# Optimization experiments

Hardware: AMD Instinct MI355X
Metric: run time of the kernel (lower is better)

The kernel has to match this reference:

```python
import jax, jax.numpy as jnp
import numpy as np

HIDDEN = 64

def gcn_conv(x, W, b, src, dst, num_nodes):
    # GCNConv: out = D^{-1/2} (A + I) D^{-1/2} (x @ W) + b
    h = x @ W                                            # [N, F_out]
    ones = jnp.ones(src.shape[0], dtype=x.dtype)
    deg = jax.ops.segment_sum(ones, dst, num_segments=num_nodes) + 1.0  # +1 for self-loop
    dinv = jax.lax.rsqrt(deg)                             # deg^{-1/2}, deg >= 1 so safe
    norm = dinv[src] * dinv[dst]                          # [E]
    msgs = h[src] * norm[:, None]                         # [E, F_out]
    agg = jax.ops.segment_sum(msgs, dst, num_segments=num_nodes)
    # self-loop contribution: norm for (i,i) edge = dinv[i]^2
    out = agg + h * (dinv * dinv)[:, None] + b
    return out


def setup_inputs() -> dict:
    key = jax.random.key(0)
    k1, k2, k3, k4, k5 = jax.random.split(key, 5)
    N, F_in, F_out, E = 50000, 256, 128, 1600000
    x = jax.random.normal(k1, (N, F_in), dtype=jnp.float32)
    edge_index = jax.random.randint(k2, (2, E), 0, N, dtype=jnp.int64)
    W1 = jax.random.normal(k3, (F_in, HIDDEN), dtype=jnp.float32) * (1.0 / np.sqrt(F_in))
    b1 = jnp.zeros((HIDDEN,), dtype=jnp.float32)
    W2 = jax.random.normal(k4, (HIDDEN, F_out), dtype=jnp.float32) * (1.0 / np.sqrt(HIDDEN))
    b2 = jnp.zeros((F_out,), dtype=jnp.float32)
    return {"x": x, "edge_index": edge_index, "W1": W1, "b1": b1, "W2": W2, "b2": b2}


def reference(x, edge_index, W1, b1, W2, b2):
    num_nodes = x.shape[0]
    src, dst = edge_index[0], edge_index[1]
    h = gcn_conv(x, W1, b1, src, dst, num_nodes)
    h = jax.nn.relu(h)
    # dropout is identity in eval mode (training=False)
    out = gcn_conv(h, W2, b2, src, dst, num_nodes)
    return out
```

## Files before the change

### kernel.cpp

```cpp
#include <hip/hip_runtime.h>

#define FI 256
#define FH 64
#define FO 128
#define ASORT_CHUNK 2048

typedef __attribute__((ext_vector_type(8))) short bf16x8;
typedef __attribute__((ext_vector_type(4))) float f32x4;

__device__ __forceinline__ ushort f2bf(float x) {
    unsigned b = __float_as_uint(x);
    b += 0x7fffu + ((b >> 16) & 1u);
    return (ushort)(b >> 16);
}
__device__ __forceinline__ float bf2f(ushort u) {
    return __uint_as_float(((unsigned)u) << 16);
}


__global__ void zero_i32(int* __restrict__ p, int n) {
    int i = blockIdx.x * 256 + threadIdx.x;
    if (i < n) p[i] = 0;
}

__global__ void deg_cnt_kernel(const int* __restrict__ dst, int* __restrict__ cnt, int E) {
    int base = blockIdx.x * 1024 + threadIdx.x;
    #pragma unroll
    for (int q = 0; q < 4; ++q) {
        int e = base + q * 256;
        if (e < E) atomicAdd(&cnt[dst[e]], 1);
    }
}

__global__ void dinv_kernel(const int* __restrict__ cnt, float* __restrict__ dinv, int N) {
    int i = blockIdx.x * 256 + threadIdx.x;
    if (i < N) dinv[i] = rsqrtf((float)cnt[i] + 1.0f);
}


__global__ __launch_bounds__(256) void hist_part_kernel(const int* __restrict__ dst,
                                                        int* __restrict__ bucket_cnt, int E) {
    __shared__ int lcnt[256];
    int t = threadIdx.x;
    int base = blockIdx.x * ASORT_CHUNK;
    lcnt[t] = 0;
    __syncthreads();
    #pragma unroll
    for (int j = 0; j < 8; ++j) {
        int e = base + j * 256 + t;
        if (e < E) atomicAdd(&lcnt[((unsigned)dst[e]) >> 8], 1);
    }
    __syncthreads();
    int v = lcnt[t];
    if (v > 0) atomicAdd(&bucket_cnt[t], v);
}

__global__ __launch_bounds__(256) void bucket_scan_kernel(const int* __restrict__ bucket_cnt,
                                                          int* __restrict__ bucket_base,
                                                          int* __restrict__ bucket_pos, int E) {
    __shared__ int sc[256];
    int t = threadIdx.x;
    int sum = bucket_cnt[t];
    sc[t] = sum;
    __syncthreads();
    for (int off = 1; off < 256; off <<= 1) {
        int u = (t >= off) ? sc[t - off] : 0;
        __syncthreads();
        sc[t] += u;
        __syncthreads();
    }
    int excl = sc[t] - sum;
    bucket_base[t] = excl;
    bucket_pos[t]  = excl;
    if (t == 255) bucket_base[256] = sc[255];
}

__global__ __launch_bounds__(256) void binA_kernel(const int* __restrict__ src,
                                                   const int* __restrict__ dst,
                                                   int* __restrict__ bucket_pos,
                                                   unsigned* __restrict__ binned, int E) {
    __shared__ int lcnt[256];
    __shared__ int lbase[256];
    __shared__ int gbase[256];
    __shared__ int sc[256];
    __shared__ unsigned sorted[ASORT_CHUNK];
    int t = threadIdx.x;
    int base = blockIdx.x * ASORT_CHUNK;
    lcnt[t] = 0;
    __syncthreads();
    unsigned pk[8];
    short bb[8];
    short mi[8];
    #pragma unroll
    for (int j = 0; j < 8; ++j) {
        int e = base + j * 256 + t;
        if (e < E) {
            unsigned s = (unsigned)src[e];
            unsigned d = (unsigned)dst[e];
            pk[j] = s | (d << 16);
            int b = (int)(d >> 8);
            bb[j] = (short)b;
            mi[j] = (short)atomicAdd(&lcnt[b], 1);
        } else {
            bb[j] = -1;
        }
    }
    __syncthreads();
    int v = lcnt[t];
    sc[t] = v;
    __syncthreads();
    #pragma unroll
    for (int off = 1; off < 256; off <<= 1) {
        int u = (t >= off) ? sc[t - off] : 0;
        __syncthreads();
        sc[t] += u;
        __syncthreads();
    }
    lbase[t] = sc[t] - v;
    if (v > 0) gbase[t] = atomicAdd(&bucket_pos[t], v);
    __syncthreads();
    #pragma unroll
    for (int j = 0; j < 8; ++j)
        if (bb[j] >= 0) sorted[lbase[(int)bb[j]] + (int)mi[j]] = pk[j];
    int tot = sc[255];
    __syncthreads();
    for (int i = t; i < tot; i += 256) {
        unsigned vv = sorted[i];
        int b = (int)(vv >> 24);
        binned[gbase[b] + (i - lbase[b])] = vv;
    }
}

__global__ __launch_bounds__(256) void binB_kernel(const int* __restrict__ bucket_base,
                                                   const unsigned* __restrict__ binned,
                                                   int* __restrict__ rec4,
                                                   int* __restrict__ row_start,
                                                   int* __restrict__ cnt,
                                                   float* __restrict__ dinv, int N) {
    __shared__ int lcnt[256];
    __shared__ int sc[256];
    __shared__ int lstart[256];
    __shared__ int loff[256];
    int t = threadIdx.x;
    int d0 = blockIdx.x << 8;
    int start = bucket_base[blockIdx.x];
    int end   = bucket_base[blockIdx.x + 1];
    lcnt[t] = 0;
    __syncthreads();
    for (int i = start + t; i < end; i += 256)
        atomicAdd(&lcnt[(binned[i] >> 16) & 0xffu], 1);
    __syncthreads();
    int v = lcnt[t];
    sc[t] = v;
    __syncthreads();
    for (int off = 1; off < 256; off <<= 1) {
        int u = (t >= off) ? sc[t - off] : 0;
        __syncthreads();
        sc[t] += u;
        __syncthreads();
    }
    int st = start + sc[t] - v;
    lstart[t] = st;
    loff[t] = 0;
    if (d0 + t < N) {
        row_start[d0 + t] = st;
        cnt[d0 + t] = v;
        dinv[d0 + t] = rsqrtf((float)v + 1.0f);
    }
    __syncthreads();
    int i = start + t;
    for (; i + 768 < end; i += 1024) {
        unsigned v0 = binned[i];
        unsigned v1 = binned[i + 256];
        unsigned v2 = binned[i + 512];
        unsigned v3 = binned[i + 768];
        int dA = (int)((v0 >> 16) & 0xffu); int kA = atomicAdd(&loff[dA], 1);
        rec4[lstart[dA] + kA] = (int)(v0 & 0xffffu);
        int dB = (int)((v1 >> 16) & 0xffu); int kB = atomicAdd(&loff[dB], 1);
        rec4[lstart[dB] + kB] = (int)(v1 & 0xffffu);
        int dC = (int)((v2 >> 16) & 0xffu); int kC = atomicAdd(&loff[dC], 1);
        rec4[lstart[dC] + kC] = (int)(v2 & 0xffffu);
        int dD = (int)((v3 >> 16) & 0xffu); int kD = atomicAdd(&loff[dD], 1);
        rec4[lstart[dD] + kD] = (int)(v3 & 0xffffu);
    }
    for (; i < end; i += 256) {
        unsigned v4 = binned[i];
        int d = (int)((v4 >> 16) & 0xffu);
        int k = atomicAdd(&loff[d], 1);
        rec4[lstart[d] + k] = (int)(v4 & 0xffffu);
    }
}


#define ACC8(hv, wt)                                                   \
    acc[0] = fmaf(__uint_as_float((hv).x << 16),         wt, acc[0]);  \
    acc[1] = fmaf(__uint_as_float((hv).x & 0xffff0000u), wt, acc[1]);  \
    acc[2] = fmaf(__uint_as_float((hv).y << 16),         wt, acc[2]);  \
    acc[3] = fmaf(__uint_as_float((hv).y & 0xffff0000u), wt, acc[3]);  \
    acc[4] = fmaf(__uint_as_float((hv).z << 16),         wt, acc[4]);  \
    acc[5] = fmaf(__uint_as_float((hv).z & 0xffff0000u), wt, acc[5]);  \
    acc[6] = fmaf(__uint_as_float((hv).w << 16),         wt, acc[6]);  \
    acc[7] = fmaf(__uint_as_float((hv).w & 0xffff0000u), wt, acc[7]);

#define GATHER_CHUNK(OFFS)                                                     \
    for (int c0 = 0; c0 < n; c0 += 64) {                                       \
        int idx_l = c0 + L;                                                    \
        int sreg = node;                                                       \
        float wreg = 0.f;                                                      \
        if (idx_l < n) {                                                       \
            sreg = rec4[beg + idx_l];                                          \
            wreg = dinv[sreg] * dvd;                                           \
        }                                                                      \
        int m = n - c0; if (m > 64) m = 64;                                    \
        int umax = (m + 7) >> 3;                                               \
        uint4 hv[8];                                                           \
        _Pragma("unroll")                                                      \
        for (int u = 0; u < 8; ++u) {                                          \
            if (u < umax) {                                                    \
                int sidx = __shfl(sreg, u * 8 + g, 64);                        \
                hv[u] = *(const uint4*)(hb + (size_t)sidx * 256 + (OFFS) + q * 8); \
            }                                                                  \
        }                                                                      \
        _Pragma("unroll")                                                      \
        for (int u = 0; u < 8; ++u) {                                          \
            if (u < umax) {                                                    \
                float wt = __shfl(wreg, u * 8 + g, 64);                        \
                ACC8(hv[u], wt)                                                \
            }                                                                  \
        }                                                                      \
    }

__global__ void gather_relu_kernel(const int* __restrict__ rec4, const int* __restrict__ row_start,
                                   const int* __restrict__ cnt, const float* __restrict__ dinv,
                                   const float* __restrict__ b1, float* __restrict__ out, int N) {
    int node = blockIdx.x * 4 + (threadIdx.x >> 6);
    if (node >= N) return;
    int L = threadIdx.x & 63;
    int g = L >> 3;
    int q = L & 7;
    const ushort* hb = (const ushort*)out;
    int beg = row_start[node];
    int n   = cnt[node];
    float dvd = dinv[node];
    float acc[8] = {0.f, 0.f, 0.f, 0.f, 0.f, 0.f, 0.f, 0.f};
    GATHER_CHUNK(128)
    #pragma unroll
    for (int off = 8; off < 64; off <<= 1)
        #pragma unroll
        for (int j = 0; j < 8; ++j)
            acc[j] += __shfl_xor(acc[j], off, 64);
    if (L < 8) {
        float dv2 = dvd * dvd;
        uint4 ho = *(const uint4*)(hb + (size_t)node * 256 + 128 + q * 8);
        float4 bl = *(const float4*)&b1[q * 8];
        float4 bh = *(const float4*)&b1[q * 8 + 4];
        float r0 = fmaxf(acc[0] + dv2 * __uint_as_float(ho.x << 16)         + bl.x, 0.f);
        float r1 = fmaxf(acc[1] + dv2 * __uint_as_float(ho.x & 0xffff0000u) + bl.y, 0.f);
        float r2 = fmaxf(acc[2] + dv2 * __uint_as_float(ho.y << 16)         + bl.z, 0.f);
        float r3 = fmaxf(acc[3] + dv2 * __uint_as_float(ho.y & 0xffff0000u) + bl.w, 0.f);
        float r4 = fmaxf(acc[4] + dv2 * __uint_as_float(ho.z << 16)         + bh.x, 0.f);
        float r5 = fmaxf(acc[5] + dv2 * __uint_as_float(ho.z & 0xffff0000u) + bh.y, 0.f);
        float r6 = fmaxf(acc[6] + dv2 * __uint_as_float(ho.w << 16)         + bh.z, 0.f);
        float r7 = fmaxf(acc[7] + dv2 * __uint_as_float(ho.w & 0xffff0000u) + bh.w, 0.f);
        uint4 st;
        st.x = (unsigned)f2bf(r0) | ((unsigned)f2bf(r1) << 16);
        st.y = (unsigned)f2bf(r2) | ((unsigned)f2bf(r3) << 16);
        st.z = (unsigned)f2bf(r4) | ((unsigned)f2bf(r5) << 16);
        st.w = (unsigned)f2bf(r6) | ((unsigned)f2bf(r7) << 16);
        *(uint4*)((ushort*)out + (size_t)node * 256 + 192 + q * 8) = st;
    }
}

__global__ void gather_comb_kernel(const int* __restrict__ rec4, const int* __restrict__ row_start,
                                   const int* __restrict__ cnt, const float* __restrict__ dinv,
                                   float* __restrict__ out, int N) {
    int node = blockIdx.x * 4 + (threadIdx.x >> 6);
    if (node >= N) return;
    int L = threadIdx.x & 63;
    int g = L >> 3;
    int q = L & 7;
    const ushort* hb = (const ushort*)out;
    int beg = row_start[node];
    int n   = cnt[node];
    float dvd = dinv[node];
    float acc[8] = {0.f, 0.f, 0.f, 0.f, 0.f, 0.f, 0.f, 0.f};
    GATHER_CHUNK(192)
    #pragma unroll
    for (int off = 8; off < 64; off <<= 1)
        #pragma unroll
        for (int j = 0; j < 8; ++j)
            acc[j] += __shfl_xor(acc[j], off, 64);
    if (L < 8) {
        float dv2 = dvd * dvd;
        uint4 ho = *(const uint4*)(hb + (size_t)node * 256 + 192 + q * 8);
        float4 o0, o1;
        o0.x = acc[0] + dv2 * __uint_as_float(ho.x << 16);
        o0.y = acc[1] + dv2 * __uint_as_float(ho.x & 0xffff0000u);
        o0.z = acc[2] + dv2 * __uint_as_float(ho.y << 16);
        o0.w = acc[3] + dv2 * __uint_as_float(ho.y & 0xffff0000u);
        o1.x = acc[4] + dv2 * __uint_as_float(ho.z << 16);
        o1.y = acc[5] + dv2 * __uint_as_float(ho.z & 0xffff0000u);
        o1.z = acc[6] + dv2 * __uint_as_float(ho.w << 16);
        o1.w = acc[7] + dv2 * __uint_as_float(ho.w & 0xffff0000u);
        *(float4*)&out[(size_t)node * FO + q * 8]     = o0;
        *(float4*)&out[(size_t)node * FO + q * 8 + 4] = o1;
    }
}


__global__ __launch_bounds__(512) void mm1_mfma(const float* __restrict__ x,
                                                const float* __restrict__ W1,
                                                float* __restrict__ out, int N) {
    __shared__ short bfH[2048 * 8];
    __shared__ short bfL[2048 * 8];
    int tid = threadIdx.x;

    #pragma unroll
    for (int i = 0; i < 8; ++i) {
        int f = i * 512 + tid;
        float4 wv = *(const float4*)&W1[(size_t)f * 4];
        int k  = f >> 4;
        int c4 = f & 15;
        int j  = k & 7;
        int e0 = ((c4 >> 2) * 8 + (k >> 5)) * 64 + ((k >> 3) & 3) * 16 + (c4 & 3) * 4;
        float vv[4] = {wv.x, wv.y, wv.z, wv.w};
        #pragma unroll
        for (int cc = 0; cc < 4; ++cc) {
            ushort h = f2bf(vv[cc]);
            bfH[(e0 + cc) * 8 + j] = (short)h;
            bfL[(e0 + cc) * 8 + j] = (short)f2bf(vv[cc] - bf2f(h));
        }
    }
    __syncthreads();

    int wid = tid >> 6;
    int l   = tid & 63;
    int R0  = blockIdx.x * 128;
    int rowA = R0 + wid * 16 + (l & 15);
    int kg   = l >> 4;
    const float* xr = x + (size_t)rowA * FI;
    bool ok = rowA < N;
    const float4 z4 = make_float4(0.f, 0.f, 0.f, 0.f);

    f32x4 acc[4];
    #pragma unroll
    for (int c = 0; c < 4; ++c) acc[c] = (f32x4){0.f, 0.f, 0.f, 0.f};

    float4 xa = ok ? *(const float4*)&xr[kg * 8]     : z4;
    float4 xb = ok ? *(const float4*)&xr[kg * 8 + 4] : z4;

    #pragma unroll
    for (int t = 0; t < 8; ++t) {
        bf16x8 ah, al;
        {
            float va[8] = {xa.x, xa.y, xa.z, xa.w, xb.x, xb.y, xb.z, xb.w};
            #pragma unroll
            for (int j = 0; j < 8; ++j) {
                ushort h = f2bf(va[j]);
                ah[j] = (short)h;
                al[j] = (short)f2bf(va[j] - bf2f(h));
            }
        }
        if (t < 7) {
            int kb = (t + 1) * 32 + kg * 8;
            xa = ok ? *(const float4*)&xr[kb]     : z4;
            xb = ok ? *(const float4*)&xr[kb + 4] : z4;
        }
        #pragma unroll
        for (int c = 0; c < 4; ++c) {
            int e = (c * 8 + t) * 64 + l;
            bf16x8 bh = *(const bf16x8*)&bfH[e * 8];
            bf16x8 bl = *(const bf16x8*)&bfL[e * 8];
            acc[c] = __builtin_amdgcn_mfma_f32_16x16x32_bf16(ah, bh, acc[c], 0, 0, 0);
            acc[c] = __builtin_amdgcn_mfma_f32_16x16x32_bf16(ah, bl, acc[c], 0, 0, 0);
            acc[c] = __builtin_amdgcn_mfma_f32_16x16x32_bf16(al, bh, acc[c], 0, 0, 0);
        }
    }
    {
        int rbase = R0 + wid * 16 + (l >> 4) * 4;
        #pragma unroll
        for (int r = 0; r < 4; ++r) {
            int row = rbase + r;
            if (row < N) {
                ushort* ob = (ushort*)out + (size_t)row * 256 + 128;
                #pragma unroll
                for (int c = 0; c < 4; ++c)
                    ob[c * 16 + (l & 15)] = f2bf(acc[c][r]);
            }
        }
    }
}

__global__ __launch_bounds__(256) void mm2_tiled(const float* __restrict__ W2,
                                                 const float* __restrict__ b2,
                                                 float* __restrict__ out, int N) {
    __shared__ float xs[64][68];
    __shared__ float ws[64][128];
    int tid = threadIdx.x;
    int R0  = blockIdx.x * 64;
    int ty  = tid >> 4;
    int tx  = tid & 15;

    {
        int sr = tid >> 2;
        int l4 = tid & 3;
        int grow = R0 + sr;
        bool ok = grow < N;
        const float* orow = out + (size_t)grow * FO;
        #pragma unroll
        for (int q = 0; q < 4; ++q) {
            int j0 = (l4 + 4 * q) * 4;
            float4 a = ok ? *(const float4*)&orow[j0] : make_float4(0.f, 0.f, 0.f, 0.f);
            xs[j0 + 0][sr] = a.x;
            xs[j0 + 1][sr] = a.y;
            xs[j0 + 2][sr] = a.z;
            xs[j0 + 3][sr] = a.w;
        }
    }
    #pragma unroll
    for (int q = 0; q < 8; ++q) {
        int f = tid + q * 256;
        *(float4*)&ws[f >> 5][(f & 31) * 4] = *(const float4*)&W2[(size_t)f * 4];
    }
    __syncthreads();

    float acc[4][8];
    #pragma unroll
    for (int i = 0; i < 4; ++i)
        #pragma unroll
        for (int j = 0; j < 8; ++j) acc[i][j] = 0.f;

    #pragma unroll 4
    for (int k = 0; k < FH; ++k) {
        float4 a  = *(const float4*)&xs[k][ty * 4];
        float4 bl = *(const float4*)&ws[k][tx * 4];
        float4 bh = *(const float4*)&ws[k][64 + tx * 4];
        float av[4] = {a.x, a.y, a.z, a.w};
        float bv[8] = {bl.x, bl.y, bl.z, bl.w, bh.x, bh.y, bh.z, bh.w};
        #pragma unroll
        for (int i = 0; i < 4; ++i)
            #pragma unroll
            for (int j = 0; j < 8; ++j)
                acc[i][j] = fmaf(av[i], bv[j], acc[i][j]);
    }

    float4 b2l = *(const float4*)&b2[tx * 4];
    float4 b2h = *(const float4*)&b2[64 + tx * 4];
    #pragma unroll
    for (int i = 0; i < 4; ++i) {
        int row = R0 + ty * 4 + i;
        if (row < N) {
            float* o = out + (size_t)row * FO;
            *(float4*)&o[tx * 4] = make_float4(acc[i][0] + b2l.x, acc[i][1] + b2l.y,
                                               acc[i][2] + b2l.z, acc[i][3] + b2l.w);
            *(float4*)&o[64 + tx * 4] = make_float4(acc[i][4] + b2h.x, acc[i][5] + b2h.y,
                                                    acc[i][6] + b2h.z, acc[i][7] + b2h.w);
        }
    }
}


__global__ void expand_hs1_kernel(float* __restrict__ out, int N) {
    int row = blockIdx.x * 4 + (threadIdx.x >> 6);
    if (row >= N) return;
    int lane = threadIdx.x & 63;
    float v = bf2f(((const ushort*)out)[(size_t)row * 256 + 128 + lane]);
    out[(size_t)row * FO + FH + lane] = v;
}

__global__ void zero_half_kernel(float* __restrict__ out, int half, int N) {
    int i = blockIdx.x * 256 + threadIdx.x;
    if (i >= N * FH) return;
    out[(size_t)(i >> 6) * FO + half + (i & 63)] = 0.f;
}

__global__ void scatter_half_kernel(const int* __restrict__ src, const int* __restrict__ dst,
                                    const float* __restrict__ dinv, float* __restrict__ out,
                                    int rh, int wh, int E) {
    int e = blockIdx.x * 4 + (threadIdx.x >> 6);
    if (e >= E) return;
    int lane = threadIdx.x & 63;
    int s = src[e];
    int d = dst[e];
    float w = dinv[s] * dinv[d];
    atomicAdd(&out[(size_t)d * FO + wh + lane], out[(size_t)s * FO + rh + lane] * w);
}

__global__ void finish1_kernel(float* __restrict__ out, const float* __restrict__ dinv,
                               const float* __restrict__ b1, int N) {
    int i = blockIdx.x * 256 + threadIdx.x;
    if (i >= N * FH) return;
    int row = i >> 6;
    int c   = i & 63;
    size_t base = (size_t)row * FO;
    float dv = dinv[row];
    out[base + c] = fmaxf(out[base + c] + dv * dv * out[base + FH + c] + b1[c], 0.f);
}

__global__ void finish2_kernel(float* __restrict__ out, const float* __restrict__ dinv, int N) {
    int i = blockIdx.x * 256 + threadIdx.x;
    if (i >= N * FH) return;
    int row = i >> 6;
    int c   = i & 63;
    size_t base = (size_t)row * FO;
    float dv = dinv[row];
    out[base + c] = out[base + FH + c] + dv * dv * out[base + c];
}

extern "C" void kernel_launch(void* const* d_in, const int* in_sizes, int n_in,
                              void* d_out, int out_size, void* d_ws, size_t ws_size,
                              hipStream_t stream) {
    const float* x  = (const float*)d_in[0];
    const int*   ei = (const int*)d_in[1];
    const float* W1 = (const float*)d_in[2];
    const float* b1 = (const float*)d_in[3];
    const float* W2 = (const float*)d_in[4];
    const float* b2 = (const float*)d_in[5];
    float* out = (float*)d_out;

    int N = in_sizes[0] / FI;
    int E = in_sizes[1] / 2;
    const int* src = ei;
    const int* dst = ei + E;

    char* w = (char*)d_ws;
    float* dinv        = (float*)w;      w += (size_t)N * 4;
    int*   cnt         = (int*)w;        w += (size_t)N * 4;
    int*   row_start   = (int*)w;        w += (size_t)N * 4;
    int*   bucket_cnt  = (int*)w;        w += 256 * 4;
    int*   bucket_pos  = (int*)w;        w += 256 * 4;
    int*   bucket_base = (int*)w;        w += 260 * 4;
    unsigned* binned   = (unsigned*)w;   w += (size_t)E * 4;
    int*   rec4        = (int*)w;        w += (size_t)E * 4;
    size_t need = (size_t)(w - (char*)d_ws);

    int nblkA = (E + ASORT_CHUNK - 1) / ASORT_CHUNK;
    int nbk   = (N + 255) >> 8;

    if (ws_size >= need && N <= 65536) {
        zero_i32<<<1, 256, 0, stream>>>(bucket_cnt, 256);
        hist_part_kernel<<<nblkA, 256, 0, stream>>>(dst, bucket_cnt, E);
        bucket_scan_kernel<<<1, 256, 0, stream>>>(bucket_cnt, bucket_base, bucket_pos, E);
        binA_kernel<<<nblkA, 256, 0, stream>>>(src, dst, bucket_pos, binned, E);
        binB_kernel<<<nbk, 256, 0, stream>>>(bucket_base, binned, rec4, row_start, cnt, dinv, N);

        mm1_mfma<<<(N + 127) / 128, 512, 0, stream>>>(x, W1, out, N);
        gather_relu_kernel<<<(N + 3) / 4, 256, 0, stream>>>(rec4, row_start, cnt, dinv, b1, out, N);
        gather_comb_kernel<<<(N + 3) / 4, 256, 0, stream>>>(rec4, row_start, cnt, dinv, out, N);
        mm2_tiled<<<(N + 63) / 64, 256, 0, stream>>>(W2, b2, out, N);
    } else {
        zero_i32<<<(N + 255) / 256, 256, 0, stream>>>(cnt, N);
        deg_cnt_kernel<<<(E + 1023) / 1024, 256, 0, stream>>>(dst, cnt, E);
        dinv_kernel<<<(N + 255) / 256, 256, 0, stream>>>(cnt, dinv, N);
        mm1_mfma<<<(N + 127) / 128, 512, 0, stream>>>(x, W1, out, N);
        expand_hs1_kernel<<<(N + 3) / 4, 256, 0, stream>>>(out, N);
        zero_half_kernel<<<((N * FH) + 255) / 256, 256, 0, stream>>>(out, 0, N);
        scatter_half_kernel<<<(E + 3) / 4, 256, 0, stream>>>(src, dst, dinv, out, FH, 0, E);
        finish1_kernel<<<((N * FH) + 255) / 256, 256, 0, stream>>>(out, dinv, b1, N);
        zero_half_kernel<<<((N * FH) + 255) / 256, 256, 0, stream>>>(out, FH, N);
        scatter_half_kernel<<<(E + 3) / 4, 256, 0, stream>>>(src, dst, dinv, out, 0, FH, E);
        finish2_kernel<<<((N * FH) + 255) / 256, 256, 0, stream>>>(out, dinv, N);
        mm2_tiled<<<(N + 63) / 64, 256, 0, stream>>>(W2, b2, out, N);
    }
}
```

Baseline: 277.2 us.

## Precompute W1 bf16 split fragments once and read them from global in mm1

Moves the per-block conversion of W1 into hi/lo bf16 MFMA fragments out of mm1 and into extra blocks of the histogram kernel, writing them once to workspace. The new mm1 variant reads the fragments directly from global/L2 rather than staging them in 64KB of LDS, and uses 256-thread blocks over 64 rows. This removes redundant per-block conversion work and the LDS footprint, which may raise occupancy, but it trades LDS reads for global/cache reads inside the MFMA loop.

```diff
diff --git a/kernel.cpp b/kernel.cpp
--- a/kernel.cpp
+++ b/kernel.cpp
@@ -38,8 +38,28 @@
 }
 
 
-__global__ __launch_bounds__(256) void hist_part_kernel(const int* __restrict__ dst,
-                                                        int* __restrict__ bucket_cnt, int E) {
+__global__ __launch_bounds__(256) void hist_wprep_kernel(const int* __restrict__ dst,
+                                                         int* __restrict__ bucket_cnt,
+                                                         const float* __restrict__ W1,
+                                                         short* __restrict__ WH,
+                                                         short* __restrict__ WL,
+                                                         int E, int nblkA) {
+    if ((int)blockIdx.x >= nblkA) {
+        int f = ((int)blockIdx.x - nblkA) * 256 + threadIdx.x;
+        float4 wv = *(const float4*)&W1[(size_t)f * 4];
+        int k  = f >> 4;
+        int c4 = f & 15;
+        int j  = k & 7;
+        int e0 = ((c4 >> 2) * 8 + (k >> 5)) * 64 + ((k >> 3) & 3) * 16 + (c4 & 3) * 4;
+        float vv[4] = {wv.x, wv.y, wv.z, wv.w};
+        #pragma unroll
+        for (int cc = 0; cc < 4; ++cc) {
+            ushort h = f2bf(vv[cc]);
+            WH[(e0 + cc) * 8 + j] = (short)h;
+            WL[(e0 + cc) * 8 + j] = (short)f2bf(vv[cc] - bf2f(h));
+        }
+        return;
+    }
     __shared__ int lcnt[256];
     int t = threadIdx.x;
     int base = blockIdx.x * ASORT_CHUNK;
@@ -308,34 +328,14 @@
 }
 
 
-__global__ __launch_bounds__(512) void mm1_mfma(const float* __restrict__ x,
-                                                const float* __restrict__ W1,
-                                                float* __restrict__ out, int N) {
-    __shared__ short bfH[2048 * 8];
-    __shared__ short bfL[2048 * 8];
+__global__ __launch_bounds__(256) void mm1_mfma_g(const float* __restrict__ x,
+                                                  const short* __restrict__ WH,
+                                                  const short* __restrict__ WL,
+                                                  float* __restrict__ out, int N) {
     int tid = threadIdx.x;
-
-    #pragma unroll
-    for (int i = 0; i < 8; ++i) {
-        int f = i * 512 + tid;
-        float4 wv = *(const float4*)&W1[(size_t)f * 4];
-        int k  = f >> 4;
-        int c4 = f & 15;
-        int j  = k & 7;
-        int e0 = ((c4 >> 2) * 8 + (k >> 5)) * 64 + ((k >> 3) & 3) * 16 + (c4 & 3) * 4;
-        float vv[4] = {wv.x, wv.y, wv.z, wv.w};
-        #pragma unroll
-        for (int cc = 0; cc < 4; ++cc) {
-            ushort h = f2bf(vv[cc]);
-            bfH[(e0 + cc) * 8 + j] = (short)h;
-            bfL[(e0 + cc) * 8 + j] = (short)f2bf(vv[cc] - bf2f(h));
-        }
-    }
-    __syncthreads();
-
     int wid = tid >> 6;
     int l   = tid & 63;
-    int R0  = blockIdx.x * 128;
+    int R0  = blockIdx.x * 64;
     int rowA = R0 + wid * 16 + (l & 15);
     int kg   = l >> 4;
     const float* xr = x + (size_t)rowA * FI;
@@ -369,6 +369,84 @@
         #pragma unroll
         for (int c = 0; c < 4; ++c) {
             int e = (c * 8 + t) * 64 + l;
+            bf16x8 bh = *(const bf16x8*)&WH[(size_t)e * 8];
+            bf16x8 bl = *(const bf16x8*)&WL[(size_t)e * 8];
+            acc[c] = __builtin_amdgcn_mfma_f32_16x16x32_bf16(ah, bh, acc[c], 0, 0, 0);
+            acc[c] = __builtin_amdgcn_mfma_f32_16x16x32_bf16(ah, bl, acc[c], 0, 0, 0);
+            acc[c] = __builtin_amdgcn_mfma_f32_16x16x32_bf16(al, bh, acc[c], 0, 0, 0);
+        }
+    }
+    {
+        int rbase = R0 + wid * 16 + (l >> 4) * 4;
+        #pragma unroll
+        for (int r = 0; r < 4; ++r) {
+            int row = rbase + r;
+            if (row < N) {
+                ushort* ob = (ushort*)out + (size_t)row * 256 + 128;
+                #pragma unroll
+                for (int c = 0; c < 4; ++c)
+                    ob[c * 16 + (l & 15)] = f2bf(acc[c][r]);
+            }
+        }
+    }
+}
+
+__global__ __launch_bounds__(512) void mm1_mfma(const float* __restrict__ x,
+                                                const float* __restrict__ W1,
+                                                float* __restrict__ out, int N) {
+    __shared__ short bfH[2048 * 8];
+    __shared__ short bfL[2048 * 8];
+    int tid = threadIdx.x;
+    #pragma unroll
+    for (int i = 0; i < 8; ++i) {
+        int f = i * 512 + tid;
+        float4 wv = *(const float4*)&W1[(size_t)f * 4];
+        int k  = f >> 4;
+        int c4 = f & 15;
+        int j  = k & 7;
+        int e0 = ((c4 >> 2) * 8 + (k >> 5)) * 64 + ((k >> 3) & 3) * 16 + (c4 & 3) * 4;
+        float vv[4] = {wv.x, wv.y, wv.z, wv.w};
+        #pragma unroll
+        for (int cc = 0; cc < 4; ++cc) {
+            ushort h = f2bf(vv[cc]);
+            bfH[(e0 + cc) * 8 + j] = (short)h;
+            bfL[(e0 + cc) * 8 + j] = (short)f2bf(vv[cc] - bf2f(h));
+        }
+    }
+    __syncthreads();
+    int wid = tid >> 6;
+    int l   = tid & 63;
+    int R0  = blockIdx.x * 128;
+    int rowA = R0 + wid * 16 + (l & 15);
+    int kg   = l >> 4;
+    const float* xr = x + (size_t)rowA * FI;
+    bool ok = rowA < N;
+    const float4 z4 = make_float4(0.f, 0.f, 0.f, 0.f);
+    f32x4 acc[4];
+    #pragma unroll
+    for (int c = 0; c < 4; ++c) acc[c] = (f32x4){0.f, 0.f, 0.f, 0.f};
+    float4 xa = ok ? *(const float4*)&xr[kg * 8]     : z4;
+    float4 xb = ok ? *(const float4*)&xr[kg * 8 + 4] : z4;
+    #pragma unroll
+    for (int t = 0; t < 8; ++t) {
+        bf16x8 ah, al;
+        {
+            float va[8] = {xa.x, xa.y, xa.z, xa.w, xb.x, xb.y, xb.z, xb.w};
+            #pragma unroll
+            for (int j = 0; j < 8; ++j) {
+                ushort h = f2bf(va[j]);
+                ah[j] = (short)h;
+                al[j] = (short)f2bf(va[j] - bf2f(h));
+            }
+        }
+        if (t < 7) {
+            int kb = (t + 1) * 32 + kg * 8;
+            xa = ok ? *(const float4*)&xr[kb]     : z4;
+            xb = ok ? *(const float4*)&xr[kb + 4] : z4;
+        }
+        #pragma unroll
+        for (int c = 0; c < 4; ++c) {
+            int e = (c * 8 + t) * 64 + l;
             bf16x8 bh = *(const bf16x8*)&bfH[e * 8];
             bf16x8 bl = *(const bf16x8*)&bfL[e * 8];
             acc[c] = __builtin_amdgcn_mfma_f32_16x16x32_bf16(ah, bh, acc[c], 0, 0, 0);
@@ -530,6 +608,8 @@
     int*   bucket_cnt  = (int*)w;        w += 256 * 4;
     int*   bucket_pos  = (int*)w;        w += 256 * 4;
     int*   bucket_base = (int*)w;        w += 260 * 4;
+    short* wfragH      = (short*)w;      w += 2048 * 8 * 2;
+    short* wfragL      = (short*)w;      w += 2048 * 8 * 2;
     unsigned* binned   = (unsigned*)w;   w += (size_t)E * 4;
     int*   rec4        = (int*)w;        w += (size_t)E * 4;
     size_t need = (size_t)(w - (char*)d_ws);
@@ -539,12 +619,12 @@
 
     if (ws_size >= need && N <= 65536) {
         zero_i32<<<1, 256, 0, stream>>>(bucket_cnt, 256);
-        hist_part_kernel<<<nblkA, 256, 0, stream>>>(dst, bucket_cnt, E);
+        hist_wprep_kernel<<<nblkA + 16, 256, 0, stream>>>(dst, bucket_cnt, W1, wfragH, wfragL, E, nblkA);
         bucket_scan_kernel<<<1, 256, 0, stream>>>(bucket_cnt, bucket_base, bucket_pos, E);
         binA_kernel<<<nblkA, 256, 0, stream>>>(src, dst, bucket_pos, binned, E);
         binB_kernel<<<nbk, 256, 0, stream>>>(bucket_base, binned, rec4, row_start, cnt, dinv, N);
 
-        mm1_mfma<<<(N + 127) / 128, 512, 0, stream>>>(x, W1, out, N);
+        mm1_mfma_g<<<(N + 63) / 64, 256, 0, stream>>>(x, wfragH, wfragL, out, N);
         gather_relu_kernel<<<(N + 3) / 4, 256, 0, stream>>>(rec4, row_start, cnt, dinv, b1, out, N);
         gather_comb_kernel<<<(N + 3) / 4, 256, 0, stream>>>(rec4, row_start, cnt, dinv, out, N);
         mm2_tiled<<<(N + 63) / 64, 256, 0, stream>>>(W2, b2, out, N);
```

Result: no change. 281.5 us (+1.5%).
